# Optimization experiments

Hardware: AMD Instinct MI355X
Metric: run time of the kernel (lower is better)

## Reference

```python
import jax, jax.numpy as jnp
import numpy as np

B, L, D = 64, 512, 768
KSIZE, PAD = 3, 1
BN_EPS = 1e-5
COS_EPS = 1e-8

def _gauss_kernel(kernel_size, sigma, k):
    X = np.linspace(-k, k, kernel_size)
    x, y = np.meshgrid(X, X)
    g = 1.0 / (2 * np.pi * sigma ** 2) * np.exp(-(x ** 2 + y ** 2) / (2 * sigma ** 2))
    return g.astype(np.float32)

def setup_inputs() -> dict:
    key = jax.random.key(0)
    k1, k2, k3, k4 = jax.random.split(key, 4)
    news = jax.random.normal(k1, (B, L, D), dtype=jnp.float32)
    post = jax.random.normal(k2, (B, L, D), dtype=jnp.float32)
    gauss_kernel = jnp.asarray(_gauss_kernel(KSIZE, 2, 1))[None, None]  # (1,1,3,3), frozen
    bn_gamma = jnp.ones((1,), jnp.float32)
    bn_beta = jnp.zeros((1,), jnp.float32)
    bound = 1.0 / np.sqrt(L)
    lin_w = jax.random.uniform(k3, (L, L), jnp.float32, -bound, bound)
    lin_b = jax.random.uniform(k4, (L,), jnp.float32, -bound, bound)
    return {"news": news, "post": post, "gauss_kernel": gauss_kernel,
            "bn_gamma": bn_gamma, "bn_beta": bn_beta, "lin_w": lin_w, "lin_b": lin_b}

def reference(news, post, gauss_kernel, bn_gamma, bn_beta, lin_w, lin_b):
    # cosine similarity along feature dim (torch eps semantics)
    nn_ = jnp.maximum(jnp.linalg.norm(news, axis=-1), COS_EPS)
    np_ = jnp.maximum(jnp.linalg.norm(post, axis=-1), COS_EPS)
    cos = jnp.sum(news * post, axis=-1) / (nn_ * np_)           # (B, L)
    # the original loop writes the same cos row into every i -> broadcast
    trans = jnp.broadcast_to(cos[:, None, :], (cos.shape[0], cos.shape[1], cos.shape[1]))
    x = trans[:, None]                                           # (B,1,L,L)
    wk = jax.lax.conv_general_dilated(
        x, gauss_kernel, window_strides=(1, 1),
        padding=[(PAD, PAD), (PAD, PAD)],
        dimension_numbers=("NCHW", "OIHW", "NCHW"))             # (B,1,L,L)
    # BatchNorm2d(1) in training mode: batch stats over (N,H,W)
    mu = jnp.mean(wk)
    var = jnp.mean((wk - mu) ** 2)
    wk = (wk - mu) * jax.lax.rsqrt(var + BN_EPS) * bn_gamma[0] + bn_beta[0]
    wk = wk[:, 0]                                                # (B,L,L)
    wk = jnp.einsum("blm,nm->bln", wk, lin_w) + lin_b            # Linear over last dim
    wk = jax.nn.softmax(wk, axis=-2).sum(axis=-1)[..., None]     # (B,L,1)
    word_feat = (wk * news).mean(axis=1)                         # (B,D)
    post_feat = (wk * post).mean(axis=1)[:, None]                # (B,1,D)
    return (word_feat, post_feat)
```

## Files before the change

kernel.cpp:

```cpp
#include <hip/hip_runtime.h>
#include <math.h>

#define NB 64
#define NL 512
#define ND 768

static constexpr float kCosEps = 1e-8f;
static constexpr double kBnEps = 1e-5;

static constexpr size_t OFF_ACC = 0;
static constexpr size_t OFF_CSN = 256;
static constexpr size_t SZ_CS   = (size_t)NB * ND * 4;
static constexpr size_t OFF_CSP = OFF_CSN + SZ_CS;
static constexpr size_t MEMSET_BYTES = OFF_CSP + SZ_CS;
static constexpr size_t OFF_COS = 393728;
static constexpr size_t SZ_BL   = (size_t)NB * NL * 4;
static constexpr size_t OFF_HI  = OFF_COS + SZ_BL;
static constexpr size_t OFF_HT  = OFF_HI + SZ_BL;
static constexpr size_t OFF_HB  = OFF_HT + SZ_BL;
static constexpr size_t OFF_ABC = OFF_HB + SZ_BL;

__device__ __forceinline__ float dot4(float4 a, float4 b) {
    return a.x * b.x + a.y * b.y + a.z * b.z + a.w * b.w;
}

__global__ __launch_bounds__(256) void k1_cos_colsum(
    const float* __restrict__ news, const float* __restrict__ post,
    float* __restrict__ cosv, float* __restrict__ csn,
    float* __restrict__ csp)
{
    __shared__ float red[8][ND];
    const int b    = blockIdx.x >> 5;
    const int t    = blockIdx.x & 31;
    const int l0   = t * 16;
    const int tid  = threadIdx.x;
    const int wave = tid >> 6;
    const int lane = tid & 63;

    const size_t rbase = ((size_t)b * NL + l0 + wave * 4) * ND;
    const float4* nr = (const float4*)(news + rbase) + lane;
    const float4* pr = (const float4*)(post + rbase) + lane;

    float4 N[4][3], P[4][3];
#pragma unroll
    for (int r = 0; r < 4; ++r)
#pragma unroll
        for (int k = 0; k < 3; ++k)
            N[r][k] = nr[r * 192 + k * 64];
#pragma unroll
    for (int r = 0; r < 4; ++r)
#pragma unroll
        for (int k = 0; k < 3; ++k)
            P[r][k] = pr[r * 192 + k * 64];

    float nn[4], pp[4], npd[4];
    float an[12], ap[12];
#pragma unroll
    for (int k = 0; k < 12; ++k) { an[k] = 0.f; ap[k] = 0.f; }
#pragma unroll
    for (int r = 0; r < 4; ++r) {
        nn[r]  = dot4(N[r][0], N[r][0]) + dot4(N[r][1], N[r][1]) + dot4(N[r][2], N[r][2]);
        pp[r]  = dot4(P[r][0], P[r][0]) + dot4(P[r][1], P[r][1]) + dot4(P[r][2], P[r][2]);
        npd[r] = dot4(N[r][0], P[r][0]) + dot4(N[r][1], P[r][1]) + dot4(N[r][2], P[r][2]);
#pragma unroll
        for (int k = 0; k < 3; ++k) {
            an[4 * k + 0] += N[r][k].x; an[4 * k + 1] += N[r][k].y;
            an[4 * k + 2] += N[r][k].z; an[4 * k + 3] += N[r][k].w;
            ap[4 * k + 0] += P[r][k].x; ap[4 * k + 1] += P[r][k].y;
            ap[4 * k + 2] += P[r][k].z; ap[4 * k + 3] += P[r][k].w;
        }
    }

#pragma unroll
    for (int m = 1; m <= 32; m <<= 1) {
#pragma unroll
        for (int r = 0; r < 4; ++r) {
            nn[r]  += __shfl_xor(nn[r], m);
            pp[r]  += __shfl_xor(pp[r], m);
            npd[r] += __shfl_xor(npd[r], m);
        }
    }
    if (lane == 0) {
#pragma unroll
        for (int r = 0; r < 4; ++r) {
            const float dn = fmaxf(sqrtf(nn[r]), kCosEps) * fmaxf(sqrtf(pp[r]), kCosEps);
            cosv[b * NL + l0 + wave * 4 + r] = npd[r] / dn;
        }
    }

    {
        float4* wn = (float4*)&red[wave][0];
        float4* wp = (float4*)&red[4 + wave][0];
        wn[lane]       = make_float4(an[0], an[1], an[2], an[3]);
        wn[lane + 64]  = make_float4(an[4], an[5], an[6], an[7]);
        wn[lane + 128] = make_float4(an[8], an[9], an[10], an[11]);
        wp[lane]       = make_float4(ap[0], ap[1], ap[2], ap[3]);
        wp[lane + 64]  = make_float4(ap[4], ap[5], ap[6], ap[7]);
        wp[lane + 128] = make_float4(ap[8], ap[9], ap[10], ap[11]);
    }
    __syncthreads();
    for (int i = tid; i < ND; i += 256) {
        float sn = red[0][i] + red[1][i] + red[2][i] + red[3][i];
        float sp = red[4][i] + red[5][i] + red[6][i] + red[7][i];
        atomicAdd(&csn[b * ND + i], sn);
        atomicAdd(&csp[b * ND + i], sp);
    }
}

__global__ __launch_bounds__(256) void k2_conv_stats(
    const float* __restrict__ cosv, const float* __restrict__ g,
    float* __restrict__ hi, float* __restrict__ ht, float* __restrict__ hb,
    double* __restrict__ acc)
{
    __shared__ float row[NL + 2];
    __shared__ double sred[8];
    const int b   = blockIdx.x;
    const int tid = threadIdx.x;
    if (tid == 0) { row[0] = 0.f; row[NL + 1] = 0.f; }
    for (int j = tid; j < NL; j += 256) row[j + 1] = cosv[b * NL + j];
    __syncthreads();

    const float ci0 = g[0] + g[3] + g[6], ci1 = g[1] + g[4] + g[7], ci2 = g[2] + g[5] + g[8];
    const float ct0 = g[3] + g[6],        ct1 = g[4] + g[7],        ct2 = g[5] + g[8];
    const float cb0 = g[0] + g[3],        cb1 = g[1] + g[4],        cb2 = g[2] + g[5];

    double s = 0.0, s2 = 0.0;
    for (int j = tid; j < NL; j += 256) {
        const float a = row[j], c = row[j + 1], d = row[j + 2];
        const float vi = ci0 * a + ci1 * c + ci2 * d;
        const float vt = ct0 * a + ct1 * c + ct2 * d;
        const float vb = cb0 * a + cb1 * c + cb2 * d;
        hi[b * NL + j] = vi; ht[b * NL + j] = vt; hb[b * NL + j] = vb;
        s  += (double)vi * (NL - 2) + (double)vt + (double)vb;
        s2 += (double)vi * vi * (NL - 2) + (double)vt * vt + (double)vb * vb;
    }
    const int lane = tid & 63, wave = tid >> 6;
#pragma unroll
    for (int m = 32; m >= 1; m >>= 1) { s += __shfl_xor(s, m); s2 += __shfl_xor(s2, m); }
    if (lane == 0) { sred[wave] = s; sred[4 + wave] = s2; }
    __syncthreads();
    if (tid == 0) {
        atomicAdd(&acc[0], sred[0] + sred[1] + sred[2] + sred[3]);
        atomicAdd(&acc[1], sred[4] + sred[5] + sred[6] + sred[7]);
    }
}

__global__ __launch_bounds__(256) void k3_linear_softmax(
    const float* __restrict__ hi, const float* __restrict__ ht,
    const float* __restrict__ hb, const float* __restrict__ W,
    const float* __restrict__ bias, const float* __restrict__ gamma,
    const float* __restrict__ beta, const double* __restrict__ acc,
    float* __restrict__ abc)
{
    __shared__ float shi[NL], sht[NL], shb[NL];
    __shared__ float sred[12];
    const int b   = blockIdx.x;
    const int tid = threadIdx.x;

    const double N   = (double)NB * NL * NL;
    const double mu  = acc[0] / N;
    const double var = acc[1] / N - mu * mu;
    const float  sc  = gamma[0] * (float)(1.0 / sqrt(var + kBnEps));
    const float  sh  = beta[0] - (float)mu * sc;

    for (int j = tid; j < NL; j += 256) {
        shi[j] = hi[b * NL + j] * sc + sh;
        sht[j] = ht[b * NL + j] * sc + sh;
        shb[j] = hb[b * NL + j] * sc + sh;
    }
    __syncthreads();

    const float4* s4i = (const float4*)shi;
    const float4* s4t = (const float4*)sht;
    const float4* s4b = (const float4*)shb;

    float sa = 0.f, st = 0.f, sb = 0.f;
    for (int n = tid; n < NL; n += 256) {
        const float4* wr = (const float4*)(W + (size_t)n * NL);
        float zi = 0.f, zt = 0.f, zb = 0.f;
        for (int m = 0; m < NL / 4; ++m) {
            const float4 w  = wr[m];
            const float4 vi = s4i[m], vt = s4t[m], vb = s4b[m];
            zi += w.x * vi.x + w.y * vi.y + w.z * vi.z + w.w * vi.w;
            zt += w.x * vt.x + w.y * vt.y + w.z * vt.z + w.w * vt.w;
            zb += w.x * vb.x + w.y * vb.y + w.z * vb.z + w.w * vb.w;
        }
        const float bv = bias[n];
        zi += bv; zt += bv; zb += bv;
        const float M  = fmaxf(zi, fmaxf(zt, zb));
        const float ei = expf(zi - M), et = expf(zt - M), eb = expf(zb - M);
        const float r  = 1.f / ((float)(NL - 2) * ei + et + eb);
        sa += ei * r; st += et * r; sb += eb * r;
    }
    const int lane = tid & 63, wave = tid >> 6;
#pragma unroll
    for (int m = 32; m >= 1; m >>= 1) {
        sa += __shfl_xor(sa, m); st += __shfl_xor(st, m); sb += __shfl_xor(sb, m);
    }
    if (lane == 0) { sred[wave * 3] = sa; sred[wave * 3 + 1] = st; sred[wave * 3 + 2] = sb; }
    __syncthreads();
    if (tid == 0) {
        abc[b * 3 + 0] = sred[0] + sred[3] + sred[6] + sred[9];
        abc[b * 3 + 1] = sred[1] + sred[4] + sred[7] + sred[10];
        abc[b * 3 + 2] = sred[2] + sred[5] + sred[8] + sred[11];
    }
}

__global__ __launch_bounds__(256) void k4_out(
    const float* __restrict__ news, const float* __restrict__ post,
    const float* __restrict__ csn, const float* __restrict__ csp,
    const float* __restrict__ abc, float* __restrict__ out)
{
    const int idx = blockIdx.x * 256 + threadIdx.x;
    if (idx >= NB * ND) return;
    const int b = idx / ND, d = idx - b * ND;
    const float a  = abc[b * 3 + 0];
    const float ct = abc[b * 3 + 1];
    const float cb = abc[b * 3 + 2];
    const float cn = csn[idx];
    const float cp = csp[idx];
    const size_t base = (size_t)b * NL * ND;
    const float n0 = news[base + d], nL = news[base + (size_t)(NL - 1) * ND + d];
    const float p0 = post[base + d], pL = post[base + (size_t)(NL - 1) * ND + d];
    const float invL = 1.f / NL;
    out[idx]           = (a * cn + (ct - a) * n0 + (cb - a) * nL) * invL;
    out[NB * ND + idx] = (a * cp + (ct - a) * p0 + (cb - a) * pL) * invL;
}

extern "C" void kernel_launch(void* const* d_in, const int* in_sizes, int n_in,
                              void* d_out, int out_size, void* d_ws, size_t ws_size,
                              hipStream_t stream) {
    const float* news     = (const float*)d_in[0];
    const float* post     = (const float*)d_in[1];
    const float* g        = (const float*)d_in[2];
    const float* bn_gamma = (const float*)d_in[3];
    const float* bn_beta  = (const float*)d_in[4];
    const float* lin_w    = (const float*)d_in[5];
    const float* lin_b    = (const float*)d_in[6];
    float* out = (float*)d_out;
    char*  ws  = (char*)d_ws;

    double* acc = (double*)(ws + OFF_ACC);
    float* csn  = (float*)(ws + OFF_CSN);
    float* csp  = (float*)(ws + OFF_CSP);
    float* cosv = (float*)(ws + OFF_COS);
    float* hi   = (float*)(ws + OFF_HI);
    float* ht   = (float*)(ws + OFF_HT);
    float* hb   = (float*)(ws + OFF_HB);
    float* abc  = (float*)(ws + OFF_ABC);

    hipMemsetAsync(ws, 0, MEMSET_BYTES, stream);

    k1_cos_colsum<<<NB * 32, 256, 0, stream>>>(news, post, cosv, csn, csp);
    k2_conv_stats<<<NB, 256, 0, stream>>>(cosv, g, hi, ht, hb, acc);
    k3_linear_softmax<<<NB, 256, 0, stream>>>(hi, ht, hb, lin_w, lin_b,
                                              bn_gamma, bn_beta, acc, abc);
    k4_out<<<192, 256, 0, stream>>>(news, post, csn, csp, abc, out);
}
```

Baseline: 87.81 us.

## Fuse output kernel into linear-softmax and double rows per colsum block

The final output kernel is folded into the linear/softmax kernel: each batch block keeps its three softmax coefficients in shared memory and writes that batch's output rows directly. This removes one launch and the workspace round trip for the coefficients. Separately, the cosine/column-sum kernel now has each block handle 32 rows instead of 16, with loads interleaved per row instead of all preloaded. That halves the number of blocks and the atomic adds into the column sums, but gives fewer blocks and less memory-level parallelism per wave.

```diff
diff --git a/kernel.cpp b/kernel.cpp
--- a/kernel.cpp
+++ b/kernel.cpp
@@ -18,7 +18,6 @@
 static constexpr size_t OFF_HI  = OFF_COS + SZ_BL;
 static constexpr size_t OFF_HT  = OFF_HI + SZ_BL;
 static constexpr size_t OFF_HB  = OFF_HT + SZ_BL;
-static constexpr size_t OFF_ABC = OFF_HB + SZ_BL;
 
 __device__ __forceinline__ float dot4(float4 a, float4 b) {
     return a.x * b.x + a.y * b.y + a.z * b.z + a.w * b.w;
@@ -30,51 +29,41 @@
     float* __restrict__ csp)
 {
     __shared__ float red[8][ND];
-    const int b    = blockIdx.x >> 5;
-    const int t    = blockIdx.x & 31;
-    const int l0   = t * 16;
+    const int b    = blockIdx.x >> 4;
+    const int t    = blockIdx.x & 15;
+    const int l0   = t * 32;
     const int tid  = threadIdx.x;
     const int wave = tid >> 6;
     const int lane = tid & 63;
 
-    const size_t rbase = ((size_t)b * NL + l0 + wave * 4) * ND;
+    const size_t rbase = ((size_t)b * NL + l0 + wave * 8) * ND;
     const float4* nr = (const float4*)(news + rbase) + lane;
     const float4* pr = (const float4*)(post + rbase) + lane;
 
-    float4 N[4][3], P[4][3];
-#pragma unroll
-    for (int r = 0; r < 4; ++r)
-#pragma unroll
-        for (int k = 0; k < 3; ++k)
-            N[r][k] = nr[r * 192 + k * 64];
-#pragma unroll
-    for (int r = 0; r < 4; ++r)
-#pragma unroll
-        for (int k = 0; k < 3; ++k)
-            P[r][k] = pr[r * 192 + k * 64];
-
-    float nn[4], pp[4], npd[4];
+    float nn[8], pp[8], npd[8];
     float an[12], ap[12];
 #pragma unroll
     for (int k = 0; k < 12; ++k) { an[k] = 0.f; ap[k] = 0.f; }
-#pragma unroll
-    for (int r = 0; r < 4; ++r) {
-        nn[r]  = dot4(N[r][0], N[r][0]) + dot4(N[r][1], N[r][1]) + dot4(N[r][2], N[r][2]);
-        pp[r]  = dot4(P[r][0], P[r][0]) + dot4(P[r][1], P[r][1]) + dot4(P[r][2], P[r][2]);
-        npd[r] = dot4(N[r][0], P[r][0]) + dot4(N[r][1], P[r][1]) + dot4(N[r][2], P[r][2]);
-#pragma unroll
-        for (int k = 0; k < 3; ++k) {
-            an[4 * k + 0] += N[r][k].x; an[4 * k + 1] += N[r][k].y;
-            an[4 * k + 2] += N[r][k].z; an[4 * k + 3] += N[r][k].w;
-            ap[4 * k + 0] += P[r][k].x; ap[4 * k + 1] += P[r][k].y;
-            ap[4 * k + 2] += P[r][k].z; ap[4 * k + 3] += P[r][k].w;
-        }
+
+#pragma unroll
+    for (int r = 0; r < 8; ++r) {
+        const float4 N0 = nr[r * 192],      N1 = nr[r * 192 + 64],  N2 = nr[r * 192 + 128];
+        const float4 P0 = pr[r * 192],      P1 = pr[r * 192 + 64],  P2 = pr[r * 192 + 128];
+        nn[r]  = dot4(N0, N0) + dot4(N1, N1) + dot4(N2, N2);
+        pp[r]  = dot4(P0, P0) + dot4(P1, P1) + dot4(P2, P2);
+        npd[r] = dot4(N0, P0) + dot4(N1, P1) + dot4(N2, P2);
+        an[0] += N0.x; an[1]  += N0.y; an[2]  += N0.z; an[3]  += N0.w;
+        an[4] += N1.x; an[5]  += N1.y; an[6]  += N1.z; an[7]  += N1.w;
+        an[8] += N2.x; an[9]  += N2.y; an[10] += N2.z; an[11] += N2.w;
+        ap[0] += P0.x; ap[1]  += P0.y; ap[2]  += P0.z; ap[3]  += P0.w;
+        ap[4] += P1.x; ap[5]  += P1.y; ap[6]  += P1.z; ap[7]  += P1.w;
+        ap[8] += P2.x; ap[9]  += P2.y; ap[10] += P2.z; ap[11] += P2.w;
     }
 
 #pragma unroll
     for (int m = 1; m <= 32; m <<= 1) {
 #pragma unroll
-        for (int r = 0; r < 4; ++r) {
+        for (int r = 0; r < 8; ++r) {
             nn[r]  += __shfl_xor(nn[r], m);
             pp[r]  += __shfl_xor(pp[r], m);
             npd[r] += __shfl_xor(npd[r], m);
@@ -82,9 +71,9 @@
     }
     if (lane == 0) {
 #pragma unroll
-        for (int r = 0; r < 4; ++r) {
+        for (int r = 0; r < 8; ++r) {
             const float dn = fmaxf(sqrtf(nn[r]), kCosEps) * fmaxf(sqrtf(pp[r]), kCosEps);
-            cosv[b * NL + l0 + wave * 4 + r] = npd[r] / dn;
+            cosv[b * NL + l0 + wave * 8 + r] = npd[r] / dn;
         }
     }
 
@@ -145,15 +134,18 @@
     }
 }
 
-__global__ __launch_bounds__(256) void k3_linear_softmax(
+__global__ __launch_bounds__(256) void k3k4_linear_softmax_out(
     const float* __restrict__ hi, const float* __restrict__ ht,
     const float* __restrict__ hb, const float* __restrict__ W,
     const float* __restrict__ bias, const float* __restrict__ gamma,
     const float* __restrict__ beta, const double* __restrict__ acc,
-    float* __restrict__ abc)
+    const float* __restrict__ csn, const float* __restrict__ csp,
+    const float* __restrict__ news, const float* __restrict__ post,
+    float* __restrict__ out)
 {
     __shared__ float shi[NL], sht[NL], shb[NL];
     __shared__ float sred[12];
+    __shared__ float abc3[3];
     const int b   = blockIdx.x;
     const int tid = threadIdx.x;
 
@@ -200,31 +192,25 @@
     if (lane == 0) { sred[wave * 3] = sa; sred[wave * 3 + 1] = st; sred[wave * 3 + 2] = sb; }
     __syncthreads();
     if (tid == 0) {
-        abc[b * 3 + 0] = sred[0] + sred[3] + sred[6] + sred[9];
-        abc[b * 3 + 1] = sred[1] + sred[4] + sred[7] + sred[10];
-        abc[b * 3 + 2] = sred[2] + sred[5] + sred[8] + sred[11];
-    }
-}
-
-__global__ __launch_bounds__(256) void k4_out(
-    const float* __restrict__ news, const float* __restrict__ post,
-    const float* __restrict__ csn, const float* __restrict__ csp,
-    const float* __restrict__ abc, float* __restrict__ out)
-{
-    const int idx = blockIdx.x * 256 + threadIdx.x;
-    if (idx >= NB * ND) return;
-    const int b = idx / ND, d = idx - b * ND;
-    const float a  = abc[b * 3 + 0];
-    const float ct = abc[b * 3 + 1];
-    const float cb = abc[b * 3 + 2];
-    const float cn = csn[idx];
-    const float cp = csp[idx];
+        abc3[0] = sred[0] + sred[3] + sred[6] + sred[9];
+        abc3[1] = sred[1] + sred[4] + sred[7] + sred[10];
+        abc3[2] = sred[2] + sred[5] + sred[8] + sred[11];
+    }
+    __syncthreads();
+
+    const float a  = abc3[0];
+    const float ct = abc3[1];
+    const float cb = abc3[2];
+    const float invL = 1.f / NL;
     const size_t base = (size_t)b * NL * ND;
-    const float n0 = news[base + d], nL = news[base + (size_t)(NL - 1) * ND + d];
-    const float p0 = post[base + d], pL = post[base + (size_t)(NL - 1) * ND + d];
-    const float invL = 1.f / NL;
-    out[idx]           = (a * cn + (ct - a) * n0 + (cb - a) * nL) * invL;
-    out[NB * ND + idx] = (a * cp + (ct - a) * p0 + (cb - a) * pL) * invL;
+    for (int d = tid; d < ND; d += 256) {
+        const float cn = csn[b * ND + d];
+        const float cp = csp[b * ND + d];
+        const float n0 = news[base + d], nL = news[base + (size_t)(NL - 1) * ND + d];
+        const float p0 = post[base + d], pL = post[base + (size_t)(NL - 1) * ND + d];
+        out[b * ND + d]           = (a * cn + (ct - a) * n0 + (cb - a) * nL) * invL;
+        out[NB * ND + b * ND + d] = (a * cp + (ct - a) * p0 + (cb - a) * pL) * invL;
+    }
 }
 
 extern "C" void kernel_launch(void* const* d_in, const int* in_sizes, int n_in,
@@ -247,13 +233,12 @@
     float* hi   = (float*)(ws + OFF_HI);
     float* ht   = (float*)(ws + OFF_HT);
     float* hb   = (float*)(ws + OFF_HB);
-    float* abc  = (float*)(ws + OFF_ABC);
 
     hipMemsetAsync(ws, 0, MEMSET_BYTES, stream);
 
-    k1_cos_colsum<<<NB * 32, 256, 0, stream>>>(news, post, cosv, csn, csp);
+    k1_cos_colsum<<<NB * 16, 256, 0, stream>>>(news, post, cosv, csn, csp);
     k2_conv_stats<<<NB, 256, 0, stream>>>(cosv, g, hi, ht, hb, acc);
-    k3_linear_softmax<<<NB, 256, 0, stream>>>(hi, ht, hb, lin_w, lin_b,
-                                              bn_gamma, bn_beta, acc, abc);
-    k4_out<<<192, 256, 0, stream>>>(news, post, csn, csp, abc, out);
-}
+    k3k4_linear_softmax_out<<<NB, 256, 0, stream>>>(hi, ht, hb, lin_w, lin_b,
+                                                    bn_gamma, bn_beta, acc,
+                                                    csn, csp, news, post, out);
+}
```

After: 101.7 us. 1.16x slower.

## Fuse conv-stats, linear-softmax and output kernels into one per-batch kernel

Applied to the files above, without the earlier changes.

Merges the three small kernels after the cosine stage into a single 64-block kernel. Each block recomputes the global BatchNorm statistics redundantly from all cosine rows instead of using atomics across a kernel boundary, then rebuilds its own conv rows, runs the linear+softmax, and writes its output slice. This removes two launches, the hi/ht/hb intermediate buffers and the atomic accumulator. In exchange every block repeats the full-batch stats pass, and the output stage now runs on only 64 blocks.

```diff
diff --git a/kernel.cpp b/kernel.cpp
--- a/kernel.cpp
+++ b/kernel.cpp
@@ -8,17 +8,11 @@
 static constexpr float kCosEps = 1e-8f;
 static constexpr double kBnEps = 1e-5;
 
-static constexpr size_t OFF_ACC = 0;
-static constexpr size_t OFF_CSN = 256;
+static constexpr size_t OFF_CSN = 0;
 static constexpr size_t SZ_CS   = (size_t)NB * ND * 4;
 static constexpr size_t OFF_CSP = OFF_CSN + SZ_CS;
 static constexpr size_t MEMSET_BYTES = OFF_CSP + SZ_CS;
-static constexpr size_t OFF_COS = 393728;
-static constexpr size_t SZ_BL   = (size_t)NB * NL * 4;
-static constexpr size_t OFF_HI  = OFF_COS + SZ_BL;
-static constexpr size_t OFF_HT  = OFF_HI + SZ_BL;
-static constexpr size_t OFF_HB  = OFF_HT + SZ_BL;
-static constexpr size_t OFF_ABC = OFF_HB + SZ_BL;
+static constexpr size_t OFF_COS = MEMSET_BYTES;
 
 __device__ __forceinline__ float dot4(float4 a, float4 b) {
     return a.x * b.x + a.y * b.y + a.z * b.z + a.w * b.w;
@@ -107,73 +101,78 @@
     }
 }
 
-__global__ __launch_bounds__(256) void k2_conv_stats(
+__global__ __launch_bounds__(256) void k234_stats_linear_out(
     const float* __restrict__ cosv, const float* __restrict__ g,
-    float* __restrict__ hi, float* __restrict__ ht, float* __restrict__ hb,
-    double* __restrict__ acc)
+    const float* __restrict__ W, const float* __restrict__ bias,
+    const float* __restrict__ gamma, const float* __restrict__ beta,
+    const float* __restrict__ csn, const float* __restrict__ csp,
+    const float* __restrict__ news, const float* __restrict__ post,
+    float* __restrict__ out)
 {
-    __shared__ float row[NL + 2];
-    __shared__ double sred[8];
-    const int b   = blockIdx.x;
-    const int tid = threadIdx.x;
-    if (tid == 0) { row[0] = 0.f; row[NL + 1] = 0.f; }
-    for (int j = tid; j < NL; j += 256) row[j + 1] = cosv[b * NL + j];
-    __syncthreads();
+    __shared__ float chunk[16][NL + 2];
+    __shared__ float shi[NL], sht[NL], shb[NL];
+    __shared__ double dred[8];
+    __shared__ float sred[12];
+    __shared__ float abc3[3];
+    __shared__ float stats[2];
+    const int b    = blockIdx.x;
+    const int tid  = threadIdx.x;
+    const int lane = tid & 63, wave = tid >> 6;
 
     const float ci0 = g[0] + g[3] + g[6], ci1 = g[1] + g[4] + g[7], ci2 = g[2] + g[5] + g[8];
     const float ct0 = g[3] + g[6],        ct1 = g[4] + g[7],        ct2 = g[5] + g[8];
     const float cb0 = g[0] + g[3],        cb1 = g[1] + g[4],        cb2 = g[2] + g[5];
 
     double s = 0.0, s2 = 0.0;
+    for (int c = 0; c < NB / 16; ++c) {
+        for (int idx = tid; idx < 16 * NL; idx += 256) {
+            const int bb = idx >> 9, j = idx & (NL - 1);
+            chunk[bb][j + 1] = cosv[(c * 16 + bb) * NL + j];
+        }
+        if (tid < 16) { chunk[tid][0] = 0.f; chunk[tid][NL + 1] = 0.f; }
+        __syncthreads();
+        for (int idx = tid; idx < 16 * NL; idx += 256) {
+            const int bb = idx >> 9, j = idx & (NL - 1);
+            const float a = chunk[bb][j], cc = chunk[bb][j + 1], d = chunk[bb][j + 2];
+            const float vi = ci0 * a + ci1 * cc + ci2 * d;
+            const float vt = ct0 * a + ct1 * cc + ct2 * d;
+            const float vb = cb0 * a + cb1 * cc + cb2 * d;
+            s  += (double)vi * (NL - 2) + (double)vt + (double)vb;
+            s2 += (double)vi * vi * (NL - 2) + (double)vt * vt + (double)vb * vb;
+        }
+        __syncthreads();
+    }
+#pragma unroll
+    for (int m = 32; m >= 1; m >>= 1) { s += __shfl_xor(s, m); s2 += __shfl_xor(s2, m); }
+    if (lane == 0) { dred[wave] = s; dred[4 + wave] = s2; }
+    __syncthreads();
+    if (tid == 0) {
+        const double S  = dred[0] + dred[1] + dred[2] + dred[3];
+        const double S2 = dred[4] + dred[5] + dred[6] + dred[7];
+        const double N  = (double)NB * NL * NL;
+        const double mu  = S / N;
+        const double var = S2 / N - mu * mu;
+        const float  sc  = gamma[0] * (float)(1.0 / sqrt(var + kBnEps));
+        stats[0] = sc;
+        stats[1] = beta[0] - (float)mu * sc;
+    }
+    __syncthreads();
+    const float sc = stats[0], sh = stats[1];
+
+    for (int j = tid; j < NL; j += 256) chunk[0][j + 1] = cosv[b * NL + j];
+    if (tid == 0) { chunk[0][0] = 0.f; chunk[0][NL + 1] = 0.f; }
+    __syncthreads();
     for (int j = tid; j < NL; j += 256) {
-        const float a = row[j], c = row[j + 1], d = row[j + 2];
-        const float vi = ci0 * a + ci1 * c + ci2 * d;
-        const float vt = ct0 * a + ct1 * c + ct2 * d;
-        const float vb = cb0 * a + cb1 * c + cb2 * d;
-        hi[b * NL + j] = vi; ht[b * NL + j] = vt; hb[b * NL + j] = vb;
-        s  += (double)vi * (NL - 2) + (double)vt + (double)vb;
-        s2 += (double)vi * vi * (NL - 2) + (double)vt * vt + (double)vb * vb;
-    }
-    const int lane = tid & 63, wave = tid >> 6;
-#pragma unroll
-    for (int m = 32; m >= 1; m >>= 1) { s += __shfl_xor(s, m); s2 += __shfl_xor(s2, m); }
-    if (lane == 0) { sred[wave] = s; sred[4 + wave] = s2; }
-    __syncthreads();
-    if (tid == 0) {
-        atomicAdd(&acc[0], sred[0] + sred[1] + sred[2] + sred[3]);
-        atomicAdd(&acc[1], sred[4] + sred[5] + sred[6] + sred[7]);
-    }
-}
-
-__global__ __launch_bounds__(256) void k3_linear_softmax(
-    const float* __restrict__ hi, const float* __restrict__ ht,
-    const float* __restrict__ hb, const float* __restrict__ W,
-    const float* __restrict__ bias, const float* __restrict__ gamma,
-    const float* __restrict__ beta, const double* __restrict__ acc,
-    float* __restrict__ abc)
-{
-    __shared__ float shi[NL], sht[NL], shb[NL];
-    __shared__ float sred[12];
-    const int b   = blockIdx.x;
-    const int tid = threadIdx.x;
-
-    const double N   = (double)NB * NL * NL;
-    const double mu  = acc[0] / N;
-    const double var = acc[1] / N - mu * mu;
-    const float  sc  = gamma[0] * (float)(1.0 / sqrt(var + kBnEps));
-    const float  sh  = beta[0] - (float)mu * sc;
-
-    for (int j = tid; j < NL; j += 256) {
-        shi[j] = hi[b * NL + j] * sc + sh;
-        sht[j] = ht[b * NL + j] * sc + sh;
-        shb[j] = hb[b * NL + j] * sc + sh;
+        const float a = chunk[0][j], cc = chunk[0][j + 1], d = chunk[0][j + 2];
+        shi[j] = (ci0 * a + ci1 * cc + ci2 * d) * sc + sh;
+        sht[j] = (ct0 * a + ct1 * cc + ct2 * d) * sc + sh;
+        shb[j] = (cb0 * a + cb1 * cc + cb2 * d) * sc + sh;
     }
     __syncthreads();
 
     const float4* s4i = (const float4*)shi;
     const float4* s4t = (const float4*)sht;
     const float4* s4b = (const float4*)shb;
-
     float sa = 0.f, st = 0.f, sb = 0.f;
     for (int n = tid; n < NL; n += 256) {
         const float4* wr = (const float4*)(W + (size_t)n * NL);
@@ -192,7 +191,6 @@
         const float r  = 1.f / ((float)(NL - 2) * ei + et + eb);
         sa += ei * r; st += et * r; sb += eb * r;
     }
-    const int lane = tid & 63, wave = tid >> 6;
 #pragma unroll
     for (int m = 32; m >= 1; m >>= 1) {
         sa += __shfl_xor(sa, m); st += __shfl_xor(st, m); sb += __shfl_xor(sb, m);
@@ -200,31 +198,25 @@
     if (lane == 0) { sred[wave * 3] = sa; sred[wave * 3 + 1] = st; sred[wave * 3 + 2] = sb; }
     __syncthreads();
     if (tid == 0) {
-        abc[b * 3 + 0] = sred[0] + sred[3] + sred[6] + sred[9];
-        abc[b * 3 + 1] = sred[1] + sred[4] + sred[7] + sred[10];
-        abc[b * 3 + 2] = sred[2] + sred[5] + sred[8] + sred[11];
-    }
-}
-
-__global__ __launch_bounds__(256) void k4_out(
-    const float* __restrict__ news, const float* __restrict__ post,
-    const float* __restrict__ csn, const float* __restrict__ csp,
-    const float* __restrict__ abc, float* __restrict__ out)
-{
-    const int idx = blockIdx.x * 256 + threadIdx.x;
-    if (idx >= NB * ND) return;
-    const int b = idx / ND, d = idx - b * ND;
-    const float a  = abc[b * 3 + 0];
-    const float ct = abc[b * 3 + 1];
-    const float cb = abc[b * 3 + 2];
-    const float cn = csn[idx];
-    const float cp = csp[idx];
+        abc3[0] = sred[0] + sred[3] + sred[6] + sred[9];
+        abc3[1] = sred[1] + sred[4] + sred[7] + sred[10];
+        abc3[2] = sred[2] + sred[5] + sred[8] + sred[11];
+    }
+    __syncthreads();
+
+    const float a  = abc3[0];
+    const float ct = abc3[1];
+    const float cb = abc3[2];
+    const float invL = 1.f / NL;
     const size_t base = (size_t)b * NL * ND;
-    const float n0 = news[base + d], nL = news[base + (size_t)(NL - 1) * ND + d];
-    const float p0 = post[base + d], pL = post[base + (size_t)(NL - 1) * ND + d];
-    const float invL = 1.f / NL;
-    out[idx]           = (a * cn + (ct - a) * n0 + (cb - a) * nL) * invL;
-    out[NB * ND + idx] = (a * cp + (ct - a) * p0 + (cb - a) * pL) * invL;
+    for (int d = tid; d < ND; d += 256) {
+        const float cn = csn[b * ND + d];
+        const float cp = csp[b * ND + d];
+        const float n0 = news[base + d], nL = news[base + (size_t)(NL - 1) * ND + d];
+        const float p0 = post[base + d], pL = post[base + (size_t)(NL - 1) * ND + d];
+        out[b * ND + d]           = (a * cn + (ct - a) * n0 + (cb - a) * nL) * invL;
+        out[NB * ND + b * ND + d] = (a * cp + (ct - a) * p0 + (cb - a) * pL) * invL;
+    }
 }
 
 extern "C" void kernel_launch(void* const* d_in, const int* in_sizes, int n_in,
@@ -240,20 +232,14 @@
     float* out = (float*)d_out;
     char*  ws  = (char*)d_ws;
 
-    double* acc = (double*)(ws + OFF_ACC);
     float* csn  = (float*)(ws + OFF_CSN);
     float* csp  = (float*)(ws + OFF_CSP);
     float* cosv = (float*)(ws + OFF_COS);
-    float* hi   = (float*)(ws + OFF_HI);
-    float* ht   = (float*)(ws + OFF_HT);
-    float* hb   = (float*)(ws + OFF_HB);
-    float* abc  = (float*)(ws + OFF_ABC);
 
     hipMemsetAsync(ws, 0, MEMSET_BYTES, stream);
 
     k1_cos_colsum<<<NB * 32, 256, 0, stream>>>(news, post, cosv, csn, csp);
-    k2_conv_stats<<<NB, 256, 0, stream>>>(cosv, g, hi, ht, hb, acc);
-    k3_linear_softmax<<<NB, 256, 0, stream>>>(hi, ht, hb, lin_w, lin_b,
-                                              bn_gamma, bn_beta, acc, abc);
-    k4_out<<<192, 256, 0, stream>>>(news, post, csn, csp, abc, out);
-}
+    k234_stats_linear_out<<<NB, 256, 0, stream>>>(cosv, g, lin_w, lin_b,
+                                                  bn_gamma, bn_beta,
+                                                  csn, csp, news, post, out);
+}
```

New measurement: 95.35 us. +8.6%, slower.
